# Kernel tuning notes

Hardware: AMD Instinct MI355X
Metric: run time of the kernel (lower is better)

## Reference

```python
import jax, jax.numpy as jnp
import numpy as np

B, L, DIM, HID, DSSH, DSSN = 2, 4096, 1024, 4096, 512, 512


def _ln(x, w, b):
    # LayerNorm over last dim, eps=1e-5 (torch default)
    m = x.mean(-1, keepdims=True)
    v = ((x - m) ** 2).mean(-1, keepdims=True)
    return (x - m) * jax.lax.rsqrt(v + 1e-5) * w + b


def _dss(x, n2_w, n2_b, LR, LI, CR, CI, D):
    # x: [B, L, dss_hidden]
    Lseq = x.shape[-2]
    xn = _ln(x, n2_w, n2_b)
    Lam = (-jnp.exp(LR) + 1j * jnp.exp(LI)).astype(jnp.complex64)        # [N]
    t = jnp.arange(Lseq, dtype=jnp.float32)
    S = jnp.exp(Lam[:, None] * t[None, :])                               # [N, L]
    Cc = (CR + 1j * CI) * ((jnp.exp(Lam) - 1.0) / Lam)                   # [H, N]
    K = jnp.einsum('hn,nl->lh', Cc, S).real                              # [L, H]
    n2 = 2 * Lseq
    Kf = jnp.fft.rfft(K, n=n2, axis=-2)                                  # [L+1, H]
    uf = jnp.fft.rfft(xn, n=n2, axis=-2)                                 # [B, L+1, H]
    y = jnp.fft.irfft(uf * Kf, n=n2, axis=-2)[..., :Lseq, :]
    return y + D * xn


def setup_inputs() -> dict:
    key = jax.random.key(0)
    ks = jax.random.split(key, 12)
    s = lambda k, sh, sc=1.0: jax.random.normal(k, sh, jnp.float32) * sc
    return dict(
        idx=s(ks[0], (B, L, DIM)),
        n1_w=jnp.ones((DIM,), jnp.float32), n1_b=jnp.zeros((DIM,), jnp.float32),
        Wxg=s(ks[1], (DIM, HID), 0.02),
        Wdin=s(ks[2], (DIM, DSSH), 0.02),
        n2_w=jnp.ones((DSSH,), jnp.float32), n2_b=jnp.zeros((DSSH,), jnp.float32),
        LR=s(ks[3], (DSSN,)), LI=s(ks[4], (DSSN,)),
        CR=s(ks[5], (DSSH, DSSN), 0.1), CI=s(ks[6], (DSSH, DSSN), 0.1),
        D=s(ks[7], (DSSH,)),
        Wgate=s(ks[8], (DSSH, HID), 0.02),
        Wout=s(ks[9], (HID, DIM), 0.02), bout=jnp.zeros((DIM,), jnp.float32),
    )


def reference(idx, n1_w, n1_b, Wxg, Wdin, n2_w, n2_b, LR, LI, CR, CI, D, Wgate, Wout, bout):
    x = _ln(idx, n1_w, n1_b)
    xg = x @ Wxg                                            # [B, L, HID]
    d = _dss(x @ Wdin, n2_w, n2_b, LR, LI, CR, CI, D)       # [B, L, DSSH]
    g = d @ Wgate                                           # [B, L, HID]
    out = (g * xg) @ Wout + bout                            # dropout is identity in eval
    return out + idx
```

## Files before the change

### kernel.cpp

```cpp
#include <hip/hip_runtime.h>
#include <math.h>


typedef unsigned short u16;
typedef unsigned int u32;
typedef __attribute__((ext_vector_type(8))) __bf16 bf16x8;
typedef __attribute__((ext_vector_type(4))) float f32x4;
typedef __attribute__((ext_vector_type(4))) u32 u32x4;

__device__ __forceinline__ u16 f2bf(float f) {
  u32 u = __float_as_uint(f);
  u32 r = u + 0x7FFFu + ((u >> 16) & 1u);
  return (u16)(r >> 16);
}
__device__ __forceinline__ float bf2f(u16 h) { return __uint_as_float(((u32)h) << 16); }

__global__ __launch_bounds__(256) void trans_conv(
    const float* __restrict__ in, u16* __restrict__ out, int K, int N) {
  __shared__ float t[32][33];
  int tx = threadIdx.x & 31, ty = threadIdx.x >> 5;
  int nb = N >> 5;
  int k0 = (blockIdx.x / nb) << 5;
  int n0 = (blockIdx.x % nb) << 5;
#pragma unroll
  for (int i = 0; i < 32; i += 8)
    t[ty + i][tx] = in[(size_t)(k0 + ty + i) * N + n0 + tx];
  __syncthreads();
#pragma unroll
  for (int i = 0; i < 32; i += 8)
    out[(size_t)(n0 + ty + i) * K + k0 + tx] = f2bf(t[tx][ty + i]);
}

__global__ __launch_bounds__(256) void trans_bf(
    const u16* __restrict__ in, u16* __restrict__ out, int R, int C) {
  __shared__ u16 t[32][34];
  int tx = threadIdx.x & 31, ty = threadIdx.x >> 5;
  int nb = C >> 5;
  int r0 = (blockIdx.x / nb) << 5;
  int c0 = (blockIdx.x % nb) << 5;
#pragma unroll
  for (int i = 0; i < 32; i += 8)
    t[ty + i][tx] = in[(size_t)(r0 + ty + i) * C + c0 + tx];
  __syncthreads();
#pragma unroll
  for (int i = 0; i < 32; i += 8)
    out[(size_t)(c0 + ty + i) * R + r0 + tx] = t[tx][ty + i];
}

template <bool BOUT>
__global__ void ln_kernel(const float* __restrict__ in, const float* __restrict__ gw,
                          const float* __restrict__ gb, void* outp, int D) {
  int row = blockIdx.x;
  int tid = threadIdx.x;
  const float4* r4 = (const float4*)(in + (size_t)row * D);
  float4 v = r4[tid];
  float s = v.x + v.y + v.z + v.w;
  float ss = fmaf(v.x, v.x, fmaf(v.y, v.y, fmaf(v.z, v.z, v.w * v.w)));
#pragma unroll
  for (int o = 32; o >= 1; o >>= 1) { s += __shfl_xor(s, o); ss += __shfl_xor(ss, o); }
  __shared__ float sa[8], sb[8];
  int nw = blockDim.x >> 6;
  if ((tid & 63) == 0) { sa[tid >> 6] = s; sb[tid >> 6] = ss; }
  __syncthreads();
  float S = 0.f, SS = 0.f;
  for (int i = 0; i < nw; ++i) { S += sa[i]; SS += sb[i]; }
  float mean = S / (float)D;
  float var = SS / (float)D - mean * mean;
  float inv = rsqrtf(var + 1e-5f);
  float4 wv = ((const float4*)gw)[tid];
  float4 bv = ((const float4*)gb)[tid];
  float o0 = (v.x - mean) * inv * wv.x + bv.x;
  float o1 = (v.y - mean) * inv * wv.y + bv.y;
  float o2 = (v.z - mean) * inv * wv.z + bv.z;
  float o3 = (v.w - mean) * inv * wv.w + bv.w;
  if (BOUT) {
    ushort4 o; o.x = f2bf(o0); o.y = f2bf(o1); o.z = f2bf(o2); o.w = f2bf(o3);
    ((ushort4*)outp)[(size_t)row * (D >> 2) + tid] = o;
  } else {
    float4 o; o.x = o0; o.y = o1; o.z = o2; o.w = o3;
    ((float4*)outp)[(size_t)row * (D >> 2) + tid] = o;
  }
}

__global__ __launch_bounds__(256) void ln_stats(
    const u16* __restrict__ xdTb, float* __restrict__ meanv, float* __restrict__ invv) {
  int lane = threadIdx.x & 63;
  int seg = threadIdx.x >> 6;
  int col = blockIdx.x * 64 + lane;
  float s = 0.f, ss = 0.f;
  const u16* p = xdTb + (size_t)(seg * 128) * 8192 + col;
#pragma unroll 8
  for (int r = 0; r < 128; ++r) {
    float v = bf2f(p[(size_t)r * 8192]);
    s += v; ss = fmaf(v, v, ss);
  }
  __shared__ float sa[4][64], sb[4][64];
  sa[seg][lane] = s; sb[seg][lane] = ss;
  __syncthreads();
  if (threadIdx.x < 64) {
    float S = sa[0][lane] + sa[1][lane] + sa[2][lane] + sa[3][lane];
    float SS = sb[0][lane] + sb[1][lane] + sb[2][lane] + sb[3][lane];
    float mean = S * (1.0f / 512.0f);
    float var = SS * (1.0f / 512.0f) - mean * mean;
    meanv[blockIdx.x * 64 + lane] = mean;
    invv[blockIdx.x * 64 + lane] = rsqrtf(var + 1e-5f);
  }
}

template <int MODE>
__global__ __launch_bounds__(256, 2) void gemm128p(
    const u16* __restrict__ A, const u16* __restrict__ Bt,
    int M, int N, int K,
    float* Cf, u16* Cb,
    const float* __restrict__ bias, const float* __restrict__ res) {
  constexpr int BUF = 16384;
  __shared__ __align__(16) u16 lds[2 * BUF];
  const int tid = threadIdx.x;
  const int lane = tid & 63;
  const int w = tid >> 6;
  const int nwg = (int)gridDim.x;
  const int cpx = nwg >> 3;
  const int bid = (nwg & 7) ? (int)blockIdx.x
                            : ((int)blockIdx.x & 7) * cpx + ((int)blockIdx.x >> 3);
  const int tiles_n = N >> 7;
  const int tm = (bid / tiles_n) << 7;
  const int tn = (bid % tiles_n) << 7;

  const int wm = w >> 1, wn = w & 1;
  const int lr = lane & 15;
  const int kq = lane >> 4;
  const int l7 = lane & 7;
  const int rsub = lane >> 3;
  const int sslot = (lane & 7) ^ rsub;
  const u16* gA = A + (size_t)(tm + w * 32 + rsub) * K + sslot * 8;
  const u16* gB = Bt + (size_t)(tn + w * 32 + rsub) * K + sslot * 8;
  auto ldsc = (__attribute__((address_space(3))) char*)lds;

#define STAGE128(kt, c)                                                                   \
  {                                                                                       \
    const size_t kof = (size_t)(kt) << 6;                                                 \
    _Pragma("unroll") for (int i = 0; i < 4; ++i) {                                       \
      u32 da = (u32)((c)*BUF + (w * 32 + i * 8) * 64) * 2u;                               \
      __builtin_amdgcn_global_load_lds(                                                   \
          (const __attribute__((address_space(1))) void*)(gA + (size_t)(i * 8) * K + kof),\
          (__attribute__((address_space(3))) void*)(ldsc + da), 16, 0, 0);                \
      __builtin_amdgcn_global_load_lds(                                                   \
          (const __attribute__((address_space(1))) void*)(gB + (size_t)(i * 8) * K + kof),\
          (__attribute__((address_space(3))) void*)(ldsc + da + 16384), 16, 0, 0);        \
    }                                                                                     \
  }

  f32x4 acc[4][4] = {};
  const int NT = K >> 6;

  STAGE128(0, 0);
  asm volatile("s_waitcnt vmcnt(0)" ::: "memory");
  __builtin_amdgcn_s_barrier();
  __builtin_amdgcn_sched_barrier(0);

  int cur = 0;
  for (int kt = 0; kt < NT; ++kt) {
    if (kt + 1 < NT) STAGE128(kt + 1, cur ^ 1);
    const u32 ab = (u32)cur * BUF;
#pragma unroll
    for (int ks = 0; ks < 2; ++ks) {
      const int slp = ((((ks << 2) | kq)) ^ l7) << 3;
      bf16x8 af[4], bv[4];
#pragma unroll
      for (int mi = 0; mi < 4; ++mi) {
        int ra = wm * 64 + mi * 16 + lr;
        af[mi] = *(const bf16x8*)&lds[ab + ra * 64 + slp];
      }
#pragma unroll
      for (int ni = 0; ni < 4; ++ni) {
        int rb = wn * 64 + ni * 16 + lr;
        bv[ni] = *(const bf16x8*)&lds[ab + 8192 + rb * 64 + slp];
      }
      __builtin_amdgcn_s_setprio(1);
#pragma unroll
      for (int mi = 0; mi < 4; ++mi)
#pragma unroll
        for (int ni = 0; ni < 4; ++ni)
          acc[mi][ni] = __builtin_amdgcn_mfma_f32_16x16x32_bf16(af[mi], bv[ni], acc[mi][ni], 0, 0, 0);
      __builtin_amdgcn_s_setprio(0);
    }
    asm volatile("s_waitcnt vmcnt(0)" ::: "memory");
    __builtin_amdgcn_s_barrier();
    __builtin_amdgcn_sched_barrier(0);
    cur ^= 1;
  }
#undef STAGE128

  float* lf = (float*)lds + w * (16 * 68);
  const int er = lane >> 2;
  const int ec = (lane & 3) << 4;
  const int gcol = tn + wn * 64 + ec;
#pragma unroll
  for (int mi = 0; mi < 4; ++mi) {
#pragma unroll
    for (int ni = 0; ni < 4; ++ni)
#pragma unroll
      for (int j = 0; j < 4; ++j)
        lf[(kq * 4 + j) * 68 + ni * 16 + lr] = acc[mi][ni][j];
    float v[16];
#pragma unroll
    for (int q = 0; q < 4; ++q)
      *(f32x4*)&v[q * 4] = *(const f32x4*)&lf[er * 68 + ec + q * 4];
    const int gr = tm + wm * 64 + mi * 16 + er;
    if (MODE == 3) {
      const float* rr = res + (size_t)gr * N + gcol;
      const float* br = bias + gcol;
      float* orr = Cf + (size_t)gr * N + gcol;
#pragma unroll
      for (int q = 0; q < 4; ++q) {
        f32x4 rv = *(const f32x4*)(rr + q * 4);
        f32x4 bv4 = *(const f32x4*)(br + q * 4);
        f32x4 ov;
        ov[0] = v[q * 4 + 0] + bv4[0] + rv[0];
        ov[1] = v[q * 4 + 1] + bv4[1] + rv[1];
        ov[2] = v[q * 4 + 2] + bv4[2] + rv[2];
        ov[3] = v[q * 4 + 3] + bv4[3] + rv[3];
        *(f32x4*)(orr + q * 4) = ov;
      }
    } else {
      u32 pk[8];
#pragma unroll
      for (int e = 0; e < 8; ++e)
        pk[e] = (u32)f2bf(v[2 * e]) | ((u32)f2bf(v[2 * e + 1]) << 16);
      u16* orr = Cb + (size_t)gr * N + gcol;
      *(u32x4*)orr = u32x4{pk[0], pk[1], pk[2], pk[3]};
      *(u32x4*)(orr + 8) = u32x4{pk[4], pk[5], pk[6], pk[7]};
    }
  }
}

__global__ __launch_bounds__(256, 2) void gemm_fuse2(
    const u16* __restrict__ A1, const u16* __restrict__ B1t, int K1,
    const u16* __restrict__ A2, const u16* __restrict__ B2t, int K2,
    int M, int N, u16* __restrict__ Cb) {
  constexpr int BUF = 16384;
  __shared__ __align__(16) u16 lds[2 * BUF];
  const int tid = threadIdx.x;
  const int lane = tid & 63;
  const int w = tid >> 6;
  const int nwg = (int)gridDim.x;
  const int cpx = nwg >> 3;
  const int bid = (nwg & 7) ? (int)blockIdx.x
                            : ((int)blockIdx.x & 7) * cpx + ((int)blockIdx.x >> 3);
  const int tiles_n = N >> 7;
  const int tm = (bid / tiles_n) << 7;
  const int tn = (bid % tiles_n) << 7;

  const int wm = w >> 1, wn = w & 1;
  const int lr = lane & 15;
  const int kq = lane >> 4;
  const int l7 = lane & 7;
  const int rsub = lane >> 3;
  const int sslot = (lane & 7) ^ rsub;
  auto ldsc = (__attribute__((address_space(3))) char*)lds;

  f32x4 acc1[4][4] = {};
  f32x4 acc2[4][4] = {};

#define STAGEF(gA, gB, K, kt, c)                                                          \
  {                                                                                       \
    const size_t kof = (size_t)(kt) << 6;                                                 \
    _Pragma("unroll") for (int i = 0; i < 4; ++i) {                                       \
      u32 da = (u32)((c)*BUF + (w * 32 + i * 8) * 64) * 2u;                               \
      __builtin_amdgcn_global_load_lds(                                                   \
          (const __attribute__((address_space(1))) void*)((gA) + (size_t)(i * 8) * (K) + kof), \
          (__attribute__((address_space(3))) void*)(ldsc + da), 16, 0, 0);                \
      __builtin_amdgcn_global_load_lds(                                                   \
          (const __attribute__((address_space(1))) void*)((gB) + (size_t)(i * 8) * (K) + kof), \
          (__attribute__((address_space(3))) void*)(ldsc + da + 16384), 16, 0, 0);        \
    }                                                                                     \
  }

#define KLOOP(gA, gB, K, ACC)                                                             \
  {                                                                                       \
    const int NT = (K) >> 6;                                                              \
    STAGEF(gA, gB, K, 0, 0);                                                              \
    asm volatile("s_waitcnt vmcnt(0)" ::: "memory");                                      \
    __builtin_amdgcn_s_barrier();                                                         \
    __builtin_amdgcn_sched_barrier(0);                                                    \
    int cur = 0;                                                                          \
    for (int kt = 0; kt < NT; ++kt) {                                                     \
      if (kt + 1 < NT) STAGEF(gA, gB, K, kt + 1, cur ^ 1);                                \
      const u32 ab = (u32)cur * BUF;                                                      \
      _Pragma("unroll") for (int ks = 0; ks < 2; ++ks) {                                  \
        const int slp = ((((ks << 2) | kq)) ^ l7) << 3;                                   \
        bf16x8 af[4], bv[4];                                                              \
        _Pragma("unroll") for (int mi = 0; mi < 4; ++mi) {                                \
          int ra = wm * 64 + mi * 16 + lr;                                                \
          af[mi] = *(const bf16x8*)&lds[ab + ra * 64 + slp];                              \
        }                                                                                 \
        _Pragma("unroll") for (int ni = 0; ni < 4; ++ni) {                                \
          int rb = wn * 64 + ni * 16 + lr;                                                \
          bv[ni] = *(const bf16x8*)&lds[ab + 8192 + rb * 64 + slp];                       \
        }                                                                                 \
        __builtin_amdgcn_s_setprio(1);                                                    \
        _Pragma("unroll") for (int mi = 0; mi < 4; ++mi)                                  \
          _Pragma("unroll") for (int ni = 0; ni < 4; ++ni)                                \
            ACC[mi][ni] = __builtin_amdgcn_mfma_f32_16x16x32_bf16(af[mi], bv[ni], ACC[mi][ni], 0, 0, 0); \
        __builtin_amdgcn_s_setprio(0);                                                    \
      }                                                                                   \
      asm volatile("s_waitcnt vmcnt(0)" ::: "memory");                                    \
      __builtin_amdgcn_s_barrier();                                                       \
      __builtin_amdgcn_sched_barrier(0);                                                  \
      cur ^= 1;                                                                           \
    }                                                                                     \
  }

  {
    const u16* gA = A1 + (size_t)(tm + w * 32 + rsub) * K1 + sslot * 8;
    const u16* gB = B1t + (size_t)(tn + w * 32 + rsub) * K1 + sslot * 8;
    KLOOP(gA, gB, K1, acc1);
  }
  {
    const u16* gA = A2 + (size_t)(tm + w * 32 + rsub) * K2 + sslot * 8;
    const u16* gB = B2t + (size_t)(tn + w * 32 + rsub) * K2 + sslot * 8;
    KLOOP(gA, gB, K2, acc2);
  }
#undef KLOOP
#undef STAGEF

#pragma unroll
  for (int mi = 0; mi < 4; ++mi)
#pragma unroll
    for (int ni = 0; ni < 4; ++ni)
#pragma unroll
      for (int j = 0; j < 4; ++j)
        acc1[mi][ni][j] *= acc2[mi][ni][j];

  float* lf = (float*)lds + w * (16 * 68);
  const int er = lane >> 2;
  const int ec = (lane & 3) << 4;
  const int gcol = tn + wn * 64 + ec;
#pragma unroll
  for (int mi = 0; mi < 4; ++mi) {
#pragma unroll
    for (int ni = 0; ni < 4; ++ni)
#pragma unroll
      for (int j = 0; j < 4; ++j)
        lf[(kq * 4 + j) * 68 + ni * 16 + lr] = acc1[mi][ni][j];
    float v[16];
#pragma unroll
    for (int q = 0; q < 4; ++q)
      *(f32x4*)&v[q * 4] = *(const f32x4*)&lf[er * 68 + ec + q * 4];
    const int gr = tm + wm * 64 + mi * 16 + er;
    u32 pk[8];
#pragma unroll
    for (int e = 0; e < 8; ++e)
      pk[e] = (u32)f2bf(v[2 * e]) | ((u32)f2bf(v[2 * e + 1]) << 16);
    u16* orr = Cb + (size_t)gr * N + gcol;
    *(u32x4*)orr = u32x4{pk[0], pk[1], pk[2], pk[3]};
    *(u32x4*)(orr + 8) = u32x4{pk[4], pk[5], pk[6], pk[7]};
  }
}

__global__ __launch_bounds__(256) void kgen_s(
    const float* __restrict__ LR, const float* __restrict__ LI, u16* __restrict__ SRSI) {
  int idx0 = blockIdx.x * 256 + threadIdx.x;
  int l = idx0 >> 10;
  int kk = idx0 & 1023;
  int n = kk & 511;
  double a = exp((double)LR[n]);
  double om = exp((double)LI[n]);
  double ld = (double)l;
  float decay = (float)exp(-a * ld);
  double th = fmod(om * ld, 6.283185307179586477);
  float c, s;
  sincosf((float)th, &s, &c);
  SRSI[idx0] = f2bf(decay * ((kk < 512) ? c : s));
}

__global__ __launch_bounds__(256) void kgen_c(
    const float* __restrict__ LR, const float* __restrict__ LI,
    const float* __restrict__ CR, const float* __restrict__ CI, u16* __restrict__ Ct) {
  int idx0 = blockIdx.x * 256 + threadIdx.x;
  int h = idx0 >> 9, n = idx0 & 511;
  float eLR = expf(LR[n]), eLI = expf(LI[n]);
  float lre = -eLR, lim = eLI;
  float er = expf(lre);
  float c, s;
  sincosf(lim, &s, &c);
  float wr = er * c - 1.0f, wi = er * s;
  float den = lre * lre + lim * lim;
  float gr = (wr * lre + wi * lim) / den;
  float gi = (wi * lre - wr * lim) / den;
  float cr = CR[(size_t)h * 512 + n], ci = CI[(size_t)h * 512 + n];
  float ccr = cr * gr - ci * gi;
  float cci = cr * gi + ci * gr;
  Ct[(size_t)h * 1024 + n] = f2bf(ccr);
  Ct[(size_t)h * 1024 + 512 + n] = f2bf(-cci);
}

__global__ __launch_bounds__(256) void twfill(float4* __restrict__ twg4) {
  int j = blockIdx.x * 256 + threadIdx.x;
  float t1 = -6.2831853071795864769f * (float)j / 8192.0f;
  float s1, c1, s2, c2;
  sincosf(t1, &s1, &c1);
  sincosf(2.0f * t1, &s2, &c2);
  twg4[j] = {c1, s1, c2, s2};
}

struct C2 { float x, y; };
__device__ __forceinline__ C2 cadd(C2 a, C2 b) { return {a.x + b.x, a.y + b.y}; }
__device__ __forceinline__ C2 csub(C2 a, C2 b) { return {a.x - b.x, a.y - b.y}; }
__device__ __forceinline__ C2 cmul(C2 a, C2 b) {
  return {a.x * b.x - a.y * b.y, a.x * b.y + a.y * b.x};
}
__device__ __forceinline__ C2 cmulni(C2 a) { return {a.y, -a.x}; }

__device__ __forceinline__ int swz(int a) {
  return a ^ ((a >> 7) & 15) ^ ((a >> 11) & 3) ^ ((a >> 2) & 8) ^ ((a >> 3) & 2) ^ ((a >> 4) & 4);
}

#define BR13(x) ((int)(__brev((u32)(x)) >> 19))
#define RS 0.70710678118654752f

__device__ __forceinline__ void dif4(C2& a, C2& b, C2& c, C2& d, float4 wv) {
  C2 w = {wv.x, wv.y}, wm = {wv.y, -wv.x}, w2 = {wv.z, wv.w};
  C2 a1 = cadd(a, c);
  C2 c1 = cmul(csub(a, c), w);
  C2 b1 = cadd(b, d);
  C2 d1 = cmul(csub(b, d), wm);
  a = cadd(a1, b1);
  b = cmul(csub(a1, b1), w2);
  c = cadd(c1, d1);
  d = cmul(csub(c1, d1), w2);
}
__device__ __forceinline__ void dit4(C2& a, C2& b, C2& c, C2& d, float4 wv) {
  C2 w = {wv.x, wv.y}, wm = {wv.y, -wv.x}, wa = {wv.z, wv.w};
  C2 t = cmul(wa, b);
  C2 a1 = cadd(a, t), b1 = csub(a, t);
  C2 u = cmul(wa, d);
  C2 c1 = cadd(c, u), d1 = csub(c, u);
  C2 v = cmul(w, c1);
  C2 xx = cmul(wm, d1);
  a = cadd(a1, v);
  c = csub(a1, v);
  b = cadd(b1, xx);
  d = csub(b1, xx);
}

template <int L>
__device__ __forceinline__ void dif16(C2* z, int tid, const float4* __restrict__ twg4) {
  const int Q = 1 << (L - 2);
  const int pos2 = tid & (Q - 1);
  const int i0 = ((tid >> (L - 2)) << (L + 2)) | pos2;
  int ad[16]; C2 x[16];
#pragma unroll
  for (int k = 0; k < 16; ++k) { ad[k] = swz(i0 + k * Q); x[k] = z[ad[k]]; }
#pragma unroll
  for (int r = 0; r < 4; ++r)
    dif4(x[r], x[r + 4], x[r + 8], x[r + 12], twg4[(pos2 + r * Q) << (11 - L)]);
  {
    float4 wv2 = twg4[pos2 << (13 - L)];
#pragma unroll
    for (int m = 0; m < 4; ++m)
      dif4(x[4 * m], x[4 * m + 1], x[4 * m + 2], x[4 * m + 3], wv2);
  }
#pragma unroll
  for (int k = 0; k < 16; ++k) z[ad[k]] = x[k];
}
template <int L>
__device__ __forceinline__ void dit16(C2* z, int tid, const float4* __restrict__ twg4) {
  const int Q = 1 << (L - 2);
  const int pos2 = tid & (Q - 1);
  const int i0 = ((tid >> (L - 2)) << (L + 2)) | pos2;
  int ad[16]; C2 x[16];
#pragma unroll
  for (int k = 0; k < 16; ++k) { ad[k] = swz(i0 + k * Q); x[k] = z[ad[k]]; }
  {
    float4 wv2 = twg4[pos2 << (13 - L)];
#pragma unroll
    for (int m = 0; m < 4; ++m)
      dit4(x[4 * m], x[4 * m + 1], x[4 * m + 2], x[4 * m + 3], wv2);
  }
#pragma unroll
  for (int r = 0; r < 4; ++r)
    dit4(x[r], x[r + 4], x[r + 8], x[r + 12], twg4[(pos2 + r * Q) << (11 - L)]);
#pragma unroll
  for (int k = 0; k < 16; ++k) z[ad[k]] = x[k];
}

template <int LOGM>
__device__ __forceinline__ void dif_pass(C2* z, int tid, const float4* __restrict__ twg4) {
  const int M4 = 1 << LOGM;
#pragma unroll
  for (int j = 0; j < 4; ++j) {
    int b = tid + j * 512;
    int pos = b & (M4 - 1);
    int i0 = ((b >> LOGM) << (LOGM + 2)) | pos;
    int ia = swz(i0), ib = swz(i0 + M4), ic = swz(i0 + 2 * M4), id = swz(i0 + 3 * M4);
    C2 a = z[ia], bb = z[ib], c = z[ic], d = z[id];
    float4 wv = twg4[pos << (11 - LOGM)];
    dif4(a, bb, c, d, wv);
    z[ia] = a; z[ib] = bb; z[ic] = c; z[id] = d;
  }
}

template <int LOGM>
__device__ __forceinline__ void dit_pass(C2* z, int tid, const float4* __restrict__ twg4) {
  const int M4 = 1 << LOGM;
#pragma unroll
  for (int j = 0; j < 4; ++j) {
    int b = tid + j * 512;
    int pos = b & (M4 - 1);
    int i0 = ((b >> LOGM) << (LOGM + 2)) | pos;
    int ia = swz(i0), ib = swz(i0 + M4), ic = swz(i0 + 2 * M4), id = swz(i0 + 3 * M4);
    C2 a = z[ia], bb = z[ib], c = z[ic], d = z[id];
    float4 wv = twg4[pos << (11 - LOGM)];
    dit4(a, bb, c, d, wv);
    z[ia] = a; z[ib] = bb; z[ic] = c; z[id] = d;
  }
}

__device__ __forceinline__ void dif_r8(C2* z, int tid) {
#pragma unroll
  for (int j = 0; j < 2; ++j) {
    int base = (tid + j * 512) << 3;
    int ad[8]; C2 x[8];
#pragma unroll
    for (int e = 0; e < 8; ++e) { ad[e] = swz(base + e); x[e] = z[ad[e]]; }
    C2 t;
    t = csub(x[0], x[4]); x[0] = cadd(x[0], x[4]); x[4] = t;
    t = csub(x[1], x[5]); x[1] = cadd(x[1], x[5]); x[5] = cmul(t, {RS, -RS});
    t = csub(x[2], x[6]); x[2] = cadd(x[2], x[6]); x[6] = cmulni(t);
    t = csub(x[3], x[7]); x[3] = cadd(x[3], x[7]); x[7] = cmul(t, {-RS, -RS});
    t = csub(x[0], x[2]); x[0] = cadd(x[0], x[2]); x[2] = t;
    t = csub(x[1], x[3]); x[1] = cadd(x[1], x[3]); x[3] = cmulni(t);
    t = csub(x[4], x[6]); x[4] = cadd(x[4], x[6]); x[6] = t;
    t = csub(x[5], x[7]); x[5] = cadd(x[5], x[7]); x[7] = cmulni(t);
    t = csub(x[0], x[1]); x[0] = cadd(x[0], x[1]); x[1] = t;
    t = csub(x[2], x[3]); x[2] = cadd(x[2], x[3]); x[3] = t;
    t = csub(x[4], x[5]); x[4] = cadd(x[4], x[5]); x[5] = t;
    t = csub(x[6], x[7]); x[6] = cadd(x[6], x[7]); x[7] = t;
#pragma unroll
    for (int e = 0; e < 8; ++e) z[ad[e]] = x[e];
  }
}

__device__ __forceinline__ void r8_fused(C2* z, int tid, const u32* __restrict__ kfr) {
#pragma unroll
  for (int j = 0; j < 2; ++j) {
    int base = (tid + j * 512) << 3;
    int ad[8]; C2 x[8];
#pragma unroll
    for (int e = 0; e < 8; ++e) { ad[e] = swz(base + e); x[e] = z[ad[e]]; }
    u32x4 k0 = *(const u32x4*)(kfr + base);
    u32x4 k1 = *(const u32x4*)(kfr + base + 4);
    u32 kw[8] = {k0[0], k0[1], k0[2], k0[3], k1[0], k1[1], k1[2], k1[3]};
    C2 t;
    t = csub(x[0], x[4]); x[0] = cadd(x[0], x[4]); x[4] = t;
    t = csub(x[1], x[5]); x[1] = cadd(x[1], x[5]); x[5] = cmul(t, {RS, -RS});
    t = csub(x[2], x[6]); x[2] = cadd(x[2], x[6]); x[6] = cmulni(t);
    t = csub(x[3], x[7]); x[3] = cadd(x[3], x[7]); x[7] = cmul(t, {-RS, -RS});
    t = csub(x[0], x[2]); x[0] = cadd(x[0], x[2]); x[2] = t;
    t = csub(x[1], x[3]); x[1] = cadd(x[1], x[3]); x[3] = cmulni(t);
    t = csub(x[4], x[6]); x[4] = cadd(x[4], x[6]); x[6] = t;
    t = csub(x[5], x[7]); x[5] = cadd(x[5], x[7]); x[7] = cmulni(t);
    t = csub(x[0], x[1]); x[0] = cadd(x[0], x[1]); x[1] = t;
    t = csub(x[2], x[3]); x[2] = cadd(x[2], x[3]); x[3] = t;
    t = csub(x[4], x[5]); x[4] = cadd(x[4], x[5]); x[5] = t;
    t = csub(x[6], x[7]); x[6] = cadd(x[6], x[7]); x[7] = t;
#pragma unroll
    for (int e = 0; e < 8; ++e) {
      C2 kf = {bf2f((u16)(kw[e] & 0xffffu)), bf2f((u16)(kw[e] >> 16))};
      C2 pr = cmul(x[e], kf);
      x[e] = {pr.x, -pr.y};
    }
    t = x[1]; x[1] = csub(x[0], t); x[0] = cadd(x[0], t);
    t = x[3]; x[3] = csub(x[2], t); x[2] = cadd(x[2], t);
    t = x[5]; x[5] = csub(x[4], t); x[4] = cadd(x[4], t);
    t = x[7]; x[7] = csub(x[6], t); x[6] = cadd(x[6], t);
    t = x[2];          x[2] = csub(x[0], t); x[0] = cadd(x[0], t);
    t = cmulni(x[3]);  x[3] = csub(x[1], t); x[1] = cadd(x[1], t);
    t = x[6];          x[6] = csub(x[4], t); x[4] = cadd(x[4], t);
    t = cmulni(x[7]);  x[7] = csub(x[5], t); x[5] = cadd(x[5], t);
    t = x[4];                    x[4] = csub(x[0], t); x[0] = cadd(x[0], t);
    t = cmul(x[5], {RS, -RS});   x[5] = csub(x[1], t); x[1] = cadd(x[1], t);
    t = cmulni(x[6]);            x[6] = csub(x[2], t); x[2] = cadd(x[2], t);
    t = cmul(x[7], {-RS, -RS});  x[7] = csub(x[3], t); x[3] = cadd(x[3], t);
#pragma unroll
    for (int e = 0; e < 8; ++e) z[ad[e]] = x[e];
  }
}

__global__ __launch_bounds__(512) void kfft2(
    const u16* __restrict__ KTb, const float4* __restrict__ twg4,
    u32* __restrict__ Kfb) {
  __shared__ C2 z[8192];
  const int g = blockIdx.x;
  const int t = threadIdx.x;
  const u16* k0r = KTb + ((size_t)(2 * g) << 12);
  const u16* k1r = KTb + ((size_t)(2 * g + 1) << 12);

  C2 x[16];
#pragma unroll
  for (int k = 0; k < 8; ++k) {
    int l = t + k * 512;
    x[k] = {bf2f(k0r[l]), bf2f(k1r[l])};
  }
#pragma unroll
  for (int k = 8; k < 16; ++k) x[k] = {0.f, 0.f};
#pragma unroll
  for (int r = 0; r < 4; ++r)
    dif4(x[r], x[r + 4], x[r + 8], x[r + 12], twg4[t + r * 512]);
  {
    float4 wv2 = twg4[t << 2];
#pragma unroll
    for (int m = 0; m < 4; ++m)
      dif4(x[4 * m], x[4 * m + 1], x[4 * m + 2], x[4 * m + 3], wv2);
  }
#pragma unroll
  for (int k = 0; k < 16; ++k) z[swz(t + k * 512)] = x[k];
  __syncthreads();

  dif16<7>(z, t, twg4);   __syncthreads();
  dif_pass<3>(z, t, twg4); __syncthreads();
  dif_r8(z, t);            __syncthreads();

  u32* o0 = Kfb + ((size_t)(2 * g) << 13);
  u32* o1 = Kfb + ((size_t)(2 * g + 1) << 13);
#pragma unroll
  for (int it = 0; it < 16; ++it) {
    int p = t + it * 512;
    int k = BR13(p);
    int km = (8192 - k) & 8191;
    int p2 = BR13(km);
    C2 Zk = z[swz(p)], Zm = z[swz(p2)];
    float f0r = 0.5f * (Zk.x + Zm.x), f0i = 0.5f * (Zk.y - Zm.y);
    float f1r = 0.5f * (Zk.y + Zm.y), f1i = 0.5f * (Zm.x - Zk.x);
    o0[p] = (u32)f2bf(f0r) | ((u32)f2bf(f0i) << 16);
    o1[p] = (u32)f2bf(f1r) | ((u32)f2bf(f1i) << 16);
  }
}

__global__ __launch_bounds__(512) void fft_conv4(
    const u16* __restrict__ xdTb, const u32* __restrict__ Kfb,
    const float* __restrict__ meanv, const float* __restrict__ invv,
    const float* __restrict__ n2w, const float* __restrict__ n2b,
    const float* __restrict__ Dv, const float4* __restrict__ twg4,
    u16* __restrict__ dT) {
  __shared__ C2 z[8192];
  const int h = blockIdx.x;
  const int t = threadIdx.x;
  const u16* xr = xdTb + ((size_t)h << 13);
  const float w2h = n2w[h], b2h = n2b[h], Dh = Dv[h];

  float xn0r[8], xn1r[8];
  C2 x[16];
#pragma unroll
  for (int k = 0; k < 8; ++k) {
    int l = t + k * 512;
    float x0 = bf2f(xr[l]);
    float x1 = bf2f(xr[4096 + l]);
    xn0r[k] = (x0 - meanv[l]) * invv[l] * w2h + b2h;
    xn1r[k] = (x1 - meanv[4096 + l]) * invv[4096 + l] * w2h + b2h;
    x[k] = {xn0r[k], xn1r[k]};
  }
#pragma unroll
  for (int k = 8; k < 16; ++k) x[k] = {0.f, 0.f};
#pragma unroll
  for (int r = 0; r < 4; ++r)
    dif4(x[r], x[r + 4], x[r + 8], x[r + 12], twg4[t + r * 512]);
  {
    float4 wv2 = twg4[t << 2];
#pragma unroll
    for (int m = 0; m < 4; ++m)
      dif4(x[4 * m], x[4 * m + 1], x[4 * m + 2], x[4 * m + 3], wv2);
  }
#pragma unroll
  for (int k = 0; k < 16; ++k) z[swz(t + k * 512)] = x[k];
  __syncthreads();

  dif16<7>(z, t, twg4);    __syncthreads();
  dif_pass<3>(z, t, twg4);  __syncthreads();
  r8_fused(z, t, Kfb + ((size_t)h << 13)); __syncthreads();
  dit_pass<3>(z, t, twg4);  __syncthreads();
  dit16<7>(z, t, twg4);     __syncthreads();

#pragma unroll
  for (int k = 0; k < 16; ++k) x[k] = z[swz(t + k * 512)];
  {
    float4 wv2 = twg4[t << 2];
#pragma unroll
    for (int m = 0; m < 4; ++m)
      dit4(x[4 * m], x[4 * m + 1], x[4 * m + 2], x[4 * m + 3], wv2);
  }
  const float sc = 1.0f / 8192.0f;
  u16* drow = dT + ((size_t)h << 13);
#pragma unroll
  for (int r = 0; r < 4; ++r) {
    float4 wv = twg4[t + r * 512];
    C2 w = {wv.x, wv.y}, wm = {wv.y, -wv.x}, wa = {wv.z, wv.w};
    C2 a = x[r], bb = x[r + 4], c = x[r + 8], d = x[r + 12];
    C2 tt = cmul(wa, bb);
    C2 a1 = cadd(a, tt), b1 = csub(a, tt);
    C2 u = cmul(wa, d);
    C2 c1 = cadd(c, u), d1 = csub(c, u);
    C2 olo = cadd(a1, cmul(w, c1));
    C2 ohi = cadd(b1, cmul(wm, d1));
    int l0 = t + r * 512;
    int l1 = t + (r + 4) * 512;
    drow[l0] = f2bf(fmaf(Dh, xn0r[r], olo.x * sc));
    drow[4096 + l0] = f2bf(fmaf(Dh, xn1r[r], -olo.y * sc));
    drow[l1] = f2bf(fmaf(Dh, xn0r[r + 4], ohi.x * sc));
    drow[4096 + l1] = f2bf(fmaf(Dh, xn1r[r + 4], -ohi.y * sc));
  }
}

extern "C" void kernel_launch(void* const* d_in, const int* in_sizes, int n_in,
                              void* d_out, int out_size, void* d_ws, size_t ws_size,
                              hipStream_t stream) {
  (void)in_sizes; (void)n_in; (void)out_size; (void)ws_size;
  const float* idx  = (const float*)d_in[0];
  const float* n1w  = (const float*)d_in[1];
  const float* n1b  = (const float*)d_in[2];
  const float* Wxg  = (const float*)d_in[3];
  const float* Wdin = (const float*)d_in[4];
  const float* n2w  = (const float*)d_in[5];
  const float* n2b  = (const float*)d_in[6];
  const float* LR   = (const float*)d_in[7];
  const float* LI   = (const float*)d_in[8];
  const float* CR   = (const float*)d_in[9];
  const float* CI   = (const float*)d_in[10];
  const float* Dv   = (const float*)d_in[11];
  const float* Wgate= (const float*)d_in[12];
  const float* Wout = (const float*)d_in[13];
  const float* bout = (const float*)d_in[14];
  float* out = (float*)d_out;

  const int Bn = 2, L = 4096, DIM = 1024, HID = 4096, H = 512;
  const int M = Bn * L;

  char* p = (char*)d_ws;
  auto alloc = [&](size_t bytes) { char* q = p; p += (bytes + 255) & ~(size_t)255; return q; };
  u16* Wxg_t   = (u16*)alloc((size_t)HID * DIM * 2);
  u16* Wdin_t  = (u16*)alloc((size_t)H * DIM * 2);
  u16* Wgate_t = (u16*)alloc((size_t)HID * H * 2);
  u16* Wout_t  = (u16*)alloc((size_t)DIM * HID * 2);
  u16* xbf     = (u16*)alloc((size_t)M * DIM * 2);
  u16* ebuf    = (u16*)alloc((size_t)M * HID * 2);
  u16* xdTb    = (u16*)alloc((size_t)H * M * 2);
  float* meanv = (float*)alloc((size_t)M * 4);
  float* invv  = (float*)alloc((size_t)M * 4);
  u16* SRSI    = (u16*)alloc((size_t)L * 1024 * 2);
  u16* Ct      = (u16*)alloc((size_t)H * 1024 * 2);
  u16* KTb     = (u16*)alloc((size_t)H * L * 2);
  u16* dTm     = (u16*)alloc((size_t)H * M * 2);
  u16* dbuf    = (u16*)alloc((size_t)M * H * 2);
  float4* twg4 = (float4*)alloc((size_t)2048 * 16);
  u32* Kfb     = (u32*)alloc((size_t)H * M * 4);

  trans_conv<<<dim3((DIM / 32) * (HID / 32)), 256, 0, stream>>>(Wxg, Wxg_t, DIM, HID);
  trans_conv<<<dim3((DIM / 32) * (H / 32)), 256, 0, stream>>>(Wdin, Wdin_t, DIM, H);
  trans_conv<<<dim3((H / 32) * (HID / 32)), 256, 0, stream>>>(Wgate, Wgate_t, H, HID);
  trans_conv<<<dim3((HID / 32) * (DIM / 32)), 256, 0, stream>>>(Wout, Wout_t, HID, DIM);
  twfill<<<dim3(8), 256, 0, stream>>>(twg4);
  ln_kernel<true><<<dim3(M), 256, 0, stream>>>(idx, n1w, n1b, xbf, DIM);
  gemm128p<1><<<dim3((H / 128) * (M / 128)), 256, 0, stream>>>(
      Wdin_t, xbf, H, M, DIM, nullptr, xdTb, nullptr, nullptr);
  ln_stats<<<dim3(M / 64), 256, 0, stream>>>(xdTb, meanv, invv);
  kgen_s<<<dim3(L * 1024 / 256), 256, 0, stream>>>(LR, LI, SRSI);
  kgen_c<<<dim3(H * 512 / 256), 256, 0, stream>>>(LR, LI, CR, CI, Ct);
  gemm128p<1><<<dim3((H / 128) * (L / 128)), 256, 0, stream>>>(
      Ct, SRSI, H, L, 1024, nullptr, KTb, nullptr, nullptr);
  kfft2<<<dim3(H / 2), 512, 0, stream>>>(KTb, twg4, Kfb);
  fft_conv4<<<dim3(H), 512, 0, stream>>>(xdTb, Kfb, meanv, invv, n2w, n2b, Dv, twg4, dTm);
  trans_bf<<<dim3((H / 32) * (M / 32)), 256, 0, stream>>>(dTm, dbuf, H, M);
  gemm_fuse2<<<dim3((M / 128) * (HID / 128)), 256, 0, stream>>>(
      xbf, Wxg_t, DIM, dbuf, Wgate_t, H, M, HID, ebuf);
  gemm128p<3><<<dim3((M / 128) * (DIM / 128)), 256, 0, stream>>>(
      ebuf, Wout_t, M, DIM, HID, out, nullptr, bout, idx);
}
```

Before: 344.1 us.

## Merge prologue kernels into one launch and co-schedule kernel GEMM with LN stats

```diff
diff --git a/kernel.cpp b/kernel.cpp
--- a/kernel.cpp
+++ b/kernel.cpp
@@ -15,13 +15,13 @@
 }
 __device__ __forceinline__ float bf2f(u16 h) { return __uint_as_float(((u32)h) << 16); }
 
-__global__ __launch_bounds__(256) void trans_conv(
-    const float* __restrict__ in, u16* __restrict__ out, int K, int N) {
-  __shared__ float t[32][33];
+__device__ __forceinline__ void trans_conv_body(
+    int bid, const float* __restrict__ in, u16* __restrict__ out, int K, int N,
+    float (*t)[33]) {
   int tx = threadIdx.x & 31, ty = threadIdx.x >> 5;
   int nb = N >> 5;
-  int k0 = (blockIdx.x / nb) << 5;
-  int n0 = (blockIdx.x % nb) << 5;
+  int k0 = (bid / nb) << 5;
+  int n0 = (bid % nb) << 5;
 #pragma unroll
   for (int i = 0; i < 32; i += 8)
     t[ty + i][tx] = in[(size_t)(k0 + ty + i) * N + n0 + tx];
@@ -31,62 +31,82 @@
     out[(size_t)(n0 + ty + i) * K + k0 + tx] = f2bf(t[tx][ty + i]);
 }
 
-__global__ __launch_bounds__(256) void trans_bf(
-    const u16* __restrict__ in, u16* __restrict__ out, int R, int C) {
-  __shared__ u16 t[32][34];
-  int tx = threadIdx.x & 31, ty = threadIdx.x >> 5;
-  int nb = C >> 5;
-  int r0 = (blockIdx.x / nb) << 5;
-  int c0 = (blockIdx.x % nb) << 5;
-#pragma unroll
-  for (int i = 0; i < 32; i += 8)
-    t[ty + i][tx] = in[(size_t)(r0 + ty + i) * C + c0 + tx];
-  __syncthreads();
-#pragma unroll
-  for (int i = 0; i < 32; i += 8)
-    out[(size_t)(c0 + ty + i) * R + r0 + tx] = t[tx][ty + i];
-}
-
-template <bool BOUT>
-__global__ void ln_kernel(const float* __restrict__ in, const float* __restrict__ gw,
-                          const float* __restrict__ gb, void* outp, int D) {
-  int row = blockIdx.x;
+__device__ __forceinline__ void ln1_body(
+    int bid, const float* __restrict__ in, const float* __restrict__ gw,
+    const float* __restrict__ gb, u16* __restrict__ outp, float* sbuf) {
+  const int D = 1024;
   int tid = threadIdx.x;
-  const float4* r4 = (const float4*)(in + (size_t)row * D);
+  const float4* r4 = (const float4*)(in + (size_t)bid * D);
   float4 v = r4[tid];
   float s = v.x + v.y + v.z + v.w;
   float ss = fmaf(v.x, v.x, fmaf(v.y, v.y, fmaf(v.z, v.z, v.w * v.w)));
 #pragma unroll
   for (int o = 32; o >= 1; o >>= 1) { s += __shfl_xor(s, o); ss += __shfl_xor(ss, o); }
-  __shared__ float sa[8], sb[8];
-  int nw = blockDim.x >> 6;
+  float* sa = sbuf;
+  float* sb = sbuf + 8;
   if ((tid & 63) == 0) { sa[tid >> 6] = s; sb[tid >> 6] = ss; }
   __syncthreads();
-  float S = 0.f, SS = 0.f;
-  for (int i = 0; i < nw; ++i) { S += sa[i]; SS += sb[i]; }
+  float S = sa[0] + sa[1] + sa[2] + sa[3];
+  float SS = sb[0] + sb[1] + sb[2] + sb[3];
   float mean = S / (float)D;
   float var = SS / (float)D - mean * mean;
   float inv = rsqrtf(var + 1e-5f);
   float4 wv = ((const float4*)gw)[tid];
   float4 bv = ((const float4*)gb)[tid];
-  float o0 = (v.x - mean) * inv * wv.x + bv.x;
-  float o1 = (v.y - mean) * inv * wv.y + bv.y;
-  float o2 = (v.z - mean) * inv * wv.z + bv.z;
-  float o3 = (v.w - mean) * inv * wv.w + bv.w;
-  if (BOUT) {
-    ushort4 o; o.x = f2bf(o0); o.y = f2bf(o1); o.z = f2bf(o2); o.w = f2bf(o3);
-    ((ushort4*)outp)[(size_t)row * (D >> 2) + tid] = o;
-  } else {
-    float4 o; o.x = o0; o.y = o1; o.z = o2; o.w = o3;
-    ((float4*)outp)[(size_t)row * (D >> 2) + tid] = o;
-  }
-}
-
-__global__ __launch_bounds__(256) void ln_stats(
-    const u16* __restrict__ xdTb, float* __restrict__ meanv, float* __restrict__ invv) {
+  ushort4 o;
+  o.x = f2bf((v.x - mean) * inv * wv.x + bv.x);
+  o.y = f2bf((v.y - mean) * inv * wv.y + bv.y);
+  o.z = f2bf((v.z - mean) * inv * wv.z + bv.z);
+  o.w = f2bf((v.w - mean) * inv * wv.w + bv.w);
+  ((ushort4*)outp)[(size_t)bid * (D >> 2) + tid] = o;
+}
+
+__device__ __forceinline__ void kgen_c_body(
+    int bid, const float* __restrict__ LR, const float* __restrict__ LI,
+    const float* __restrict__ CR, const float* __restrict__ CI, u16* __restrict__ Ct) {
+  int idx0 = bid * 256 + threadIdx.x;
+  int h = idx0 >> 9, n = idx0 & 511;
+  float eLR = expf(LR[n]), eLI = expf(LI[n]);
+  float lre = -eLR, lim = eLI;
+  float er = expf(lre);
+  float c, s;
+  sincosf(lim, &s, &c);
+  float wr = er * c - 1.0f, wi = er * s;
+  float den = lre * lre + lim * lim;
+  float gr = (wr * lre + wi * lim) / den;
+  float gi = (wi * lre - wr * lim) / den;
+  float cr = CR[(size_t)h * 512 + n], ci = CI[(size_t)h * 512 + n];
+  float ccr = cr * gr - ci * gi;
+  float cci = cr * gi + ci * gr;
+  Ct[(size_t)h * 1024 + n] = f2bf(ccr);
+  Ct[(size_t)h * 1024 + 512 + n] = f2bf(-cci);
+}
+
+__device__ __forceinline__ void twfill_body(int bid, float4* __restrict__ twg4) {
+  int j = bid * 256 + threadIdx.x;
+  float t1 = -6.2831853071795864769f * (float)j / 8192.0f;
+  float s1, c1, s2, c2;
+  sincosf(t1, &s1, &c1);
+  sincosf(2.0f * t1, &s2, &c2);
+  twg4[j] = {c1, s1, c2, s2};
+}
+
+__device__ __forceinline__ void tab_body(
+    int bid, const float* __restrict__ LR, const float* __restrict__ LI,
+    double* __restrict__ aexp, double* __restrict__ fexp) {
+  int n = bid * 256 + threadIdx.x;
+  if (n < 512) {
+    aexp[n] = exp((double)LR[n]);
+    fexp[n] = exp((double)LI[n]) * 0.15915494309189533577;
+  }
+}
+
+__device__ __forceinline__ void ln_stats_body(
+    int bid, const u16* __restrict__ xdTb, float* __restrict__ meanv,
+    float* __restrict__ invv, float* sbuf) {
   int lane = threadIdx.x & 63;
   int seg = threadIdx.x >> 6;
-  int col = blockIdx.x * 64 + lane;
+  int col = bid * 64 + lane;
   float s = 0.f, ss = 0.f;
   const u16* p = xdTb + (size_t)(seg * 128) * 8192 + col;
 #pragma unroll 8
@@ -94,34 +114,31 @@
     float v = bf2f(p[(size_t)r * 8192]);
     s += v; ss = fmaf(v, v, ss);
   }
-  __shared__ float sa[4][64], sb[4][64];
-  sa[seg][lane] = s; sb[seg][lane] = ss;
+  float* sa = sbuf;
+  float* sb = sbuf + 256;
+  sa[seg * 64 + lane] = s; sb[seg * 64 + lane] = ss;
   __syncthreads();
   if (threadIdx.x < 64) {
-    float S = sa[0][lane] + sa[1][lane] + sa[2][lane] + sa[3][lane];
-    float SS = sb[0][lane] + sb[1][lane] + sb[2][lane] + sb[3][lane];
+    float S = sa[lane] + sa[64 + lane] + sa[128 + lane] + sa[192 + lane];
+    float SS = sb[lane] + sb[64 + lane] + sb[128 + lane] + sb[192 + lane];
     float mean = S * (1.0f / 512.0f);
     float var = SS * (1.0f / 512.0f) - mean * mean;
-    meanv[blockIdx.x * 64 + lane] = mean;
-    invv[blockIdx.x * 64 + lane] = rsqrtf(var + 1e-5f);
+    meanv[bid * 64 + lane] = mean;
+    invv[bid * 64 + lane] = rsqrtf(var + 1e-5f);
   }
 }
 
 template <int MODE>
-__global__ __launch_bounds__(256, 2) void gemm128p(
-    const u16* __restrict__ A, const u16* __restrict__ Bt,
-    int M, int N, int K,
-    float* Cf, u16* Cb,
-    const float* __restrict__ bias, const float* __restrict__ res) {
+__device__ __forceinline__ void gemm128p_body(
+    int bid0, int nwg, const u16* __restrict__ A, const u16* __restrict__ Bt,
+    int M, int N, int K, float* Cf, u16* Cb,
+    const float* __restrict__ bias, const float* __restrict__ res, u16* lds) {
   constexpr int BUF = 16384;
-  __shared__ __align__(16) u16 lds[2 * BUF];
   const int tid = threadIdx.x;
   const int lane = tid & 63;
   const int w = tid >> 6;
-  const int nwg = (int)gridDim.x;
   const int cpx = nwg >> 3;
-  const int bid = (nwg & 7) ? (int)blockIdx.x
-                            : ((int)blockIdx.x & 7) * cpx + ((int)blockIdx.x >> 3);
+  const int bid = (nwg & 7) ? bid0 : (bid0 & 7) * cpx + (bid0 >> 3);
   const int tiles_n = N >> 7;
   const int tm = (bid / tiles_n) << 7;
   const int tn = (bid % tiles_n) << 7;
@@ -232,6 +249,88 @@
       *(u32x4*)(orr + 8) = u32x4{pk[4], pk[5], pk[6], pk[7]};
     }
   }
+}
+
+
+__global__ __launch_bounds__(256) void mega1(
+    const float* __restrict__ idxf, const float* __restrict__ n1w, const float* __restrict__ n1b,
+    const float* __restrict__ Wxg, const float* __restrict__ Wdin,
+    const float* __restrict__ Wgate, const float* __restrict__ Wout,
+    u16* __restrict__ Wxg_t, u16* __restrict__ Wdin_t,
+    u16* __restrict__ Wgate_t, u16* __restrict__ Wout_t,
+    u16* __restrict__ xbf, float4* __restrict__ twg4,
+    const float* __restrict__ LR, const float* __restrict__ LI,
+    const float* __restrict__ CR, const float* __restrict__ CI,
+    u16* __restrict__ Ct, double* __restrict__ aexp, double* __restrict__ fexp) {
+  __shared__ __align__(16) char smem[4352];
+  int b = (int)blockIdx.x;
+  if (b < 8192) { ln1_body(b, idxf, n1w, n1b, xbf, (float*)smem); return; }
+  b -= 8192;
+  if (b < 4096) { trans_conv_body(b, Wxg, Wxg_t, 1024, 4096, (float(*)[33])smem); return; }
+  b -= 4096;
+  if (b < 4096) { trans_conv_body(b, Wout, Wout_t, 4096, 1024, (float(*)[33])smem); return; }
+  b -= 4096;
+  if (b < 2048) { trans_conv_body(b, Wgate, Wgate_t, 512, 4096, (float(*)[33])smem); return; }
+  b -= 2048;
+  if (b < 512) { trans_conv_body(b, Wdin, Wdin_t, 1024, 512, (float(*)[33])smem); return; }
+  b -= 512;
+  if (b < 1024) { kgen_c_body(b, LR, LI, CR, CI, Ct); return; }
+  b -= 1024;
+  if (b < 8) { twfill_body(b, twg4); return; }
+  b -= 8;
+  tab_body(b, LR, LI, aexp, fexp);
+}
+
+__global__ __launch_bounds__(256) void kgen_s2(
+    const double* __restrict__ aexp, const double* __restrict__ fexp,
+    u16* __restrict__ SRSI) {
+  int idx0 = (int)blockIdx.x * 256 + threadIdx.x;
+  int l = idx0 >> 10;
+  int kk = idx0 & 1023;
+  int n = kk & 511;
+  double fl = fexp[n] * (double)l;
+  float rev = (float)(fl - floor(fl));
+  float tri = (kk < 512) ? __builtin_amdgcn_cosf(rev) : __builtin_amdgcn_sinf(rev);
+  float al = (float)aexp[n] * (float)l;
+  SRSI[idx0] = f2bf(expf(-al) * tri);
+}
+
+template <int MODE>
+__global__ __launch_bounds__(256, 2) void gemm128p(
+    const u16* __restrict__ A, const u16* __restrict__ Bt,
+    int M, int N, int K,
+    float* Cf, u16* Cb,
+    const float* __restrict__ bias, const float* __restrict__ res) {
+  __shared__ __align__(16) u16 lds[2 * 16384];
+  gemm128p_body<MODE>((int)blockIdx.x, (int)gridDim.x, A, Bt, M, N, K, Cf, Cb, bias, res, lds);
+}
+
+__global__ __launch_bounds__(256, 2) void l3mix(
+    const u16* __restrict__ Ct, const u16* __restrict__ SRSI, u16* __restrict__ KTb,
+    const u16* __restrict__ xdTb, float* __restrict__ meanv, float* __restrict__ invv) {
+  __shared__ __align__(16) u16 lds[2 * 16384];
+  int b = (int)blockIdx.x;
+  if (b < 128) {
+    gemm128p_body<1>(b, 128, Ct, SRSI, 512, 4096, 1024, nullptr, KTb, nullptr, nullptr, lds);
+  } else {
+    ln_stats_body(b - 128, xdTb, meanv, invv, (float*)lds);
+  }
+}
+
+__global__ __launch_bounds__(256) void trans_bf(
+    const u16* __restrict__ in, u16* __restrict__ out, int R, int C) {
+  __shared__ u16 t[32][34];
+  int tx = threadIdx.x & 31, ty = threadIdx.x >> 5;
+  int nb = C >> 5;
+  int r0 = (blockIdx.x / nb) << 5;
+  int c0 = (blockIdx.x % nb) << 5;
+#pragma unroll
+  for (int i = 0; i < 32; i += 8)
+    t[ty + i][tx] = in[(size_t)(r0 + ty + i) * C + c0 + tx];
+  __syncthreads();
+#pragma unroll
+  for (int i = 0; i < 32; i += 8)
+    out[(size_t)(c0 + ty + i) * R + r0 + tx] = t[tx][ty + i];
 }
 
 __global__ __launch_bounds__(256, 2) void gemm_fuse2(
@@ -358,52 +457,6 @@
   }
 }
 
-__global__ __launch_bounds__(256) void kgen_s(
-    const float* __restrict__ LR, const float* __restrict__ LI, u16* __restrict__ SRSI) {
-  int idx0 = blockIdx.x * 256 + threadIdx.x;
-  int l = idx0 >> 10;
-  int kk = idx0 & 1023;
-  int n = kk & 511;
-  double a = exp((double)LR[n]);
-  double om = exp((double)LI[n]);
-  double ld = (double)l;
-  float decay = (float)exp(-a * ld);
-  double th = fmod(om * ld, 6.283185307179586477);
-  float c, s;
-  sincosf((float)th, &s, &c);
-  SRSI[idx0] = f2bf(decay * ((kk < 512) ? c : s));
-}
-
-__global__ __launch_bounds__(256) void kgen_c(
-    const float* __restrict__ LR, const float* __restrict__ LI,
-    const float* __restrict__ CR, const float* __restrict__ CI, u16* __restrict__ Ct) {
-  int idx0 = blockIdx.x * 256 + threadIdx.x;
-  int h = idx0 >> 9, n = idx0 & 511;
-  float eLR = expf(LR[n]), eLI = expf(LI[n]);
-  float lre = -eLR, lim = eLI;
-  float er = expf(lre);
-  float c, s;
-  sincosf(lim, &s, &c);
-  float wr = er * c - 1.0f, wi = er * s;
-  float den = lre * lre + lim * lim;
-  float gr = (wr * lre + wi * lim) / den;
-  float gi = (wi * lre - wr * lim) / den;
-  float cr = CR[(size_t)h * 512 + n], ci = CI[(size_t)h * 512 + n];
-  float ccr = cr * gr - ci * gi;
-  float cci = cr * gi + ci * gr;
-  Ct[(size_t)h * 1024 + n] = f2bf(ccr);
-  Ct[(size_t)h * 1024 + 512 + n] = f2bf(-cci);
-}
-
-__global__ __launch_bounds__(256) void twfill(float4* __restrict__ twg4) {
-  int j = blockIdx.x * 256 + threadIdx.x;
-  float t1 = -6.2831853071795864769f * (float)j / 8192.0f;
-  float s1, c1, s2, c2;
-  sincosf(t1, &s1, &c1);
-  sincosf(2.0f * t1, &s2, &c2);
-  twg4[j] = {c1, s1, c2, s2};
-}
-
 struct C2 { float x, y; };
 __device__ __forceinline__ C2 cadd(C2 a, C2 b) { return {a.x + b.x, a.y + b.y}; }
 __device__ __forceinline__ C2 csub(C2 a, C2 b) { return {a.x - b.x, a.y - b.y}; }
@@ -733,8 +786,8 @@
   const float* bout = (const float*)d_in[14];
   float* out = (float*)d_out;
 
-  const int Bn = 2, L = 4096, DIM = 1024, HID = 4096, H = 512;
-  const int M = Bn * L;
+  const int L = 4096, DIM = 1024, HID = 4096, H = 512;
+  const int M = 8192;
 
   char* p = (char*)d_ws;
   auto alloc = [&](size_t bytes) { char* q = p; p += (bytes + 255) & ~(size_t)255; return q; };
@@ -754,20 +807,16 @@
   u16* dbuf    = (u16*)alloc((size_t)M * H * 2);
   float4* twg4 = (float4*)alloc((size_t)2048 * 16);
   u32* Kfb     = (u32*)alloc((size_t)H * M * 4);
-
-  trans_conv<<<dim3((DIM / 32) * (HID / 32)), 256, 0, stream>>>(Wxg, Wxg_t, DIM, HID);
-  trans_conv<<<dim3((DIM / 32) * (H / 32)), 256, 0, stream>>>(Wdin, Wdin_t, DIM, H);
-  trans_conv<<<dim3((H / 32) * (HID / 32)), 256, 0, stream>>>(Wgate, Wgate_t, H, HID);
-  trans_conv<<<dim3((HID / 32) * (DIM / 32)), 256, 0, stream>>>(Wout, Wout_t, HID, DIM);
-  twfill<<<dim3(8), 256, 0, stream>>>(twg4);
-  ln_kernel<true><<<dim3(M), 256, 0, stream>>>(idx, n1w, n1b, xbf, DIM);
+  double* aexp = (double*)alloc((size_t)512 * 8);
+  double* fexp = (double*)alloc((size_t)512 * 8);
+
+  mega1<<<dim3(8192 + 4096 + 4096 + 2048 + 512 + 1024 + 8 + 2), 256, 0, stream>>>(
+      idx, n1w, n1b, Wxg, Wdin, Wgate, Wout,
+      Wxg_t, Wdin_t, Wgate_t, Wout_t, xbf, twg4, LR, LI, CR, CI, Ct, aexp, fexp);
+  kgen_s2<<<dim3(L * 1024 / 256), 256, 0, stream>>>(aexp, fexp, SRSI);
   gemm128p<1><<<dim3((H / 128) * (M / 128)), 256, 0, stream>>>(
       Wdin_t, xbf, H, M, DIM, nullptr, xdTb, nullptr, nullptr);
-  ln_stats<<<dim3(M / 64), 256, 0, stream>>>(xdTb, meanv, invv);
-  kgen_s<<<dim3(L * 1024 / 256), 256, 0, stream>>>(LR, LI, SRSI);
-  kgen_c<<<dim3(H * 512 / 256), 256, 0, stream>>>(LR, LI, CR, CI, Ct);
-  gemm128p<1><<<dim3((H / 128) * (L / 128)), 256, 0, stream>>>(
-      Ct, SRSI, H, L, 1024, nullptr, KTb, nullptr, nullptr);
+  l3mix<<<dim3(256), 256, 0, stream>>>(Ct, SRSI, KTb, xdTb, meanv, invv);
   kfft2<<<dim3(H / 2), 512, 0, stream>>>(KTb, twg4, Kfb);
   fft_conv4<<<dim3(H), 512, 0, stream>>>(xdTb, Kfb, meanv, invv, n2w, n2b, Dv, twg4, dTm);
   trans_bf<<<dim3((H / 32) * (M / 32)), 256, 0, stream>>>(dTm, dbuf, H, M);
```

New measurement: 311.6 us. 9.5% less time.
